# Kernel optimization log

Measured on AMD Instinct MI355X. Metric: run time of the kernel, lower is better.

The kernel has to match this reference:

```python
import jax, jax.numpy as jnp
import numpy as np
import math

NUM_HEAD = 4
GROUPS = 32
EPS = 1e-5


def setup_inputs() -> dict:
    key = jax.random.key(0)
    k1, k2, k3 = jax.random.split(key, 3)
    B, C, H, W = 2, 256, 64, 64
    x = jax.random.normal(k1, (B, C, H, W), dtype=jnp.float32)
    gn_w = jnp.ones((C,), dtype=jnp.float32)
    gn_b = jnp.zeros((C,), dtype=jnp.float32)
    # scaling_init 'u' with scale=1: bound = sqrt(3*2/(fan_in+fan_out))
    fan = (C + 3 * C) / 2
    bound_qkv = math.sqrt(3.0 / fan)
    qkv_w = jax.random.uniform(k2, (3 * C, C), dtype=jnp.float32, minval=-bound_qkv, maxval=bound_qkv)
    bound_o = math.sqrt(3e-10 / C)
    o_w = jax.random.uniform(k3, (C, C), dtype=jnp.float32, minval=-bound_o, maxval=bound_o)
    o_b = jnp.zeros((C,), dtype=jnp.float32)
    return {"x": x, "gn_w": gn_w, "gn_b": gn_b, "qkv_w": qkv_w, "o_w": o_w, "o_b": o_b}


def _group_norm(x, w, b):
    B, C, H, W = x.shape
    xg = x.reshape(B, GROUPS, C // GROUPS, H, W)
    mean = xg.mean(axis=(2, 3, 4), keepdims=True)
    var = xg.var(axis=(2, 3, 4), keepdims=True)
    xn = ((xg - mean) * jax.lax.rsqrt(var + EPS)).reshape(B, C, H, W)
    return xn * w[None, :, None, None] + b[None, :, None, None]


def reference(x, gn_w, gn_b, qkv_w, o_w, o_b):
    B, C, H, W = x.shape
    hd = C // NUM_HEAD
    S = H * W
    norm = _group_norm(x, gn_w, gn_b)
    # 1x1 conv (no bias) == channel matmul
    qkv = jnp.einsum('oc,bchw->bohw', qkv_w, norm)
    qkv = qkv.reshape(B, NUM_HEAD, 3 * hd, S)
    q, k, v = jnp.split(qkv, 3, axis=2)  # each [B, nh, hd, S]
    scale = 1.0 / math.sqrt(C)  # note: sqrt(C), not sqrt(head_dim), per source
    attn = jnp.einsum('bncs,bnct->bnst', q, k) * scale  # [B, nh, S, S]
    attn = jax.nn.softmax(attn, axis=-1)
    out = jnp.einsum('bnst,bnct->bncs', attn, v).reshape(B, C, H, W)
    out = jnp.einsum('oc,bchw->bohw', o_w, out) + o_b[None, :, None, None]
    return out + x
```

## Files before the change

kernel.cpp:

```cpp
#include <hip/hip_runtime.h>
#include <hip/hip_bf16.h>

typedef __hip_bfloat16 bf16;
typedef short short8 __attribute__((ext_vector_type(8)));
typedef float f32x4 __attribute__((ext_vector_type(4)));

__device__ __forceinline__ float b2f(bf16 v) { return __bfloat162float(v); }

__device__ __forceinline__ unsigned short f2bf(float x) {
  unsigned u = __builtin_bit_cast(unsigned, x);
  unsigned r = u + 0x7fffu + ((u >> 16) & 1u);
  return (unsigned short)(r >> 16);
}
__device__ __forceinline__ unsigned pk2(float a, float b) {
  return (unsigned)f2bf(a) | ((unsigned)f2bf(b) << 16);
}
__device__ __forceinline__ unsigned pk2t(float a, float b) {
  return __builtin_amdgcn_perm(__builtin_bit_cast(unsigned, b),
                               __builtin_bit_cast(unsigned, a), 0x07060302u);
}
__device__ __forceinline__ float rd(const void* p, size_t i, int is32) {
  return is32 ? ((const float*)p)[i] : b2f(((const bf16*)p)[i]);
}
__device__ __forceinline__ float blo(unsigned w) {
  return __builtin_bit_cast(float, w << 16);
}
__device__ __forceinline__ float bhi(unsigned w) {
  return __builtin_bit_cast(float, w & 0xffff0000u);
}
__device__ __forceinline__ float fexp2(float x) {
  return __builtin_amdgcn_exp2f(x);
}

#define CQ 0.09016844005556022f

__global__ void __launch_bounds__(256) detect_kernel(const void* __restrict__ x,
                                                     int* __restrict__ flag) {
  __shared__ int cnt[256];
  const bf16* xb = (const bf16*)x;
  int c = 0;
  for (int i = threadIdx.x; i < 4096; i += 256) {
    float v = fabsf(b2f(xb[2 * i]));
    if (v >= 0.0009765625f && v <= 1024.0f) c++;
  }
  cnt[threadIdx.x] = c;
  __syncthreads();
  for (int off = 128; off > 0; off >>= 1) {
    if (threadIdx.x < off) cnt[threadIdx.x] += cnt[threadIdx.x + off];
    __syncthreads();
  }
  if (threadIdx.x == 0) *flag = (cnt[0] < 2048) ? 1 : 0;
}

__global__ void __launch_bounds__(256) pre1_kernel(
    const void* __restrict__ x, const void* __restrict__ gn_w,
    const void* __restrict__ gn_b, const int* __restrict__ flag,
    float* __restrict__ scale, float* __restrict__ shift,
    short* __restrict__ xT) {
  __shared__ __align__(16) float F[64][72];
  const int t = threadIdx.x;
  const int is32 = *flag;
  if (blockIdx.x < 512) {
    const int bx = blockIdx.x;
    const int b = bx >> 8, rest = bx & 255;
    const int s0 = (rest >> 2) * 64, c0 = (rest & 3) * 64;
    if (is32) {
      const float* xp = (const float*)x;
#pragma unroll
      for (int k = 0; k < 4; k++) {
        int idx = k * 256 + t, cl = idx >> 4, c4 = idx & 15;
        float4 v = *(const float4*)&xp[(size_t)(b * 256 + c0 + cl) * 4096 + s0 +
                                       c4 * 4];
        *(float4*)&F[cl][c4 * 4] = v;
      }
    } else {
      const bf16* xp = (const bf16*)x;
#pragma unroll
      for (int k = 0; k < 2; k++) {
        int idx = k * 256 + t, cl = idx >> 3, c8 = idx & 7;
        uint4 u = *(const uint4*)&xp[(size_t)(b * 256 + c0 + cl) * 4096 + s0 +
                                     c8 * 8];
        float4 f0, f1;
        f0.x = blo(u.x); f0.y = bhi(u.x); f0.z = blo(u.y); f0.w = bhi(u.y);
        f1.x = blo(u.z); f1.y = bhi(u.z); f1.z = blo(u.w); f1.w = bhi(u.w);
        *(float4*)&F[cl][c8 * 8] = f0;
        *(float4*)&F[cl][c8 * 8 + 4] = f1;
      }
    }
    __syncthreads();
#pragma unroll
    for (int k = 0; k < 8; k++) {
      int idx = k * 256 + t;
      int sl = idx >> 5, c2 = (idx & 31) * 2;
      unsigned u = pk2(F[c2][sl], F[c2 + 1][sl]);
      *(unsigned*)&xT[((size_t)b * 4096 + s0 + sl) * 256 + c0 + c2] = u;
    }
  } else {
    const int idx0 = blockIdx.x - 512;
    const int b = idx0 >> 5, g = idx0 & 31;
    const size_t base = (size_t)(b * 256 + g * 8) * 4096;
    float s = 0.f, ss = 0.f;
    if (is32) {
      const float4* p = (const float4*)((const float*)x + base);
      for (int i = t; i < 8192; i += 256) {
        float4 v = p[i];
        s += (v.x + v.y) + (v.z + v.w);
        ss += v.x * v.x + v.y * v.y + v.z * v.z + v.w * v.w;
      }
    } else {
      const uint4* p = (const uint4*)((const bf16*)x + base);
      for (int i = t; i < 4096; i += 256) {
        uint4 u = p[i];
#pragma unroll
        for (int k = 0; k < 4; k++) {
          unsigned w = (&u.x)[k];
          float lo = blo(w), hi = bhi(w);
          s += lo + hi;
          ss += lo * lo + hi * hi;
        }
      }
    }
    float* rs = &F[0][0];
    float* rq = rs + 256;
    rs[t] = s;
    rq[t] = ss;
    __syncthreads();
    for (int off = 128; off > 0; off >>= 1) {
      if (t < off) {
        rs[t] += rs[t + off];
        rq[t] += rq[t + off];
      }
      __syncthreads();
    }
    if (t < 8) {
      const float inv_n = 1.f / 32768.f;
      float mean = rs[0] * inv_n;
      float var = rq[0] * inv_n - mean * mean;
      float rstd = rsqrtf(var + 1e-5f);
      int c = g * 8 + t;
      float sc = rd(gn_w, c, is32) * rstd;
      scale[b * 256 + c] = sc;
      shift[b * 256 + c] = rd(gn_b, c, is32) - mean * sc;
    }
  }
}

__global__ void __launch_bounds__(256) pre2_kernel(
    const void* __restrict__ qkv_w, const void* __restrict__ o_w,
    const void* __restrict__ o_b, const float* __restrict__ scale,
    const float* __restrict__ shift, const int* __restrict__ flag,
    short* __restrict__ W2, float* __restrict__ bias2, short* __restrict__ owb,
    float* __restrict__ obf) {
  const int is32 = *flag;
  if (blockIdx.x < 192) {
    const int b = blockIdx.y;
    const int o = blockIdx.x * 4 + (threadIdx.x >> 6);
    const int lane = threadIdx.x & 63;
    const float f = (o % 192 < 64) ? CQ : 1.0f;
    float w[4], acc = 0.f;
#pragma unroll
    for (int k = 0; k < 4; k++) {
      int c = lane * 4 + k;
      w[k] = rd(qkv_w, (size_t)o * 256 + c, is32);
      acc += w[k] * shift[b * 256 + c];
      w[k] = w[k] * scale[b * 256 + c] * f;
    }
#pragma unroll
    for (int m = 1; m < 64; m <<= 1) acc += __shfl_xor(acc, m);
    if (lane == 0) bias2[b * 768 + o] = acc * f;
    uint2 u;
    u.x = pk2(w[0], w[1]);
    u.y = pk2(w[2], w[3]);
    *(uint2*)&W2[((size_t)b * 768 + o) * 256 + lane * 4] = u;
  } else if (blockIdx.y == 0) {
    int bx = blockIdx.x - 192;
    int i = (bx * 256 + threadIdx.x) * 4;
    uint2 u;
    u.x = pk2(rd(o_w, i, is32), rd(o_w, i + 1, is32));
    u.y = pk2(rd(o_w, i + 2, is32), rd(o_w, i + 3, is32));
    *(uint2*)&owb[i] = u;
    if (bx == 0) obf[threadIdx.x] = rd(o_b, threadIdx.x, is32);
  }
}

__global__ void __launch_bounds__(256) gemm_qkv_kernel(
    const short* __restrict__ xT, const short* __restrict__ W2,
    const float* __restrict__ bias2, short* __restrict__ qT,
    short* __restrict__ kF, short* __restrict__ vF) {
  __shared__ __align__(16) short lds[128 * 72 + 64 * 72];
  short* At = lds;
  short* Bt = lds + 128 * 72;
  const int t = threadIdx.x;
  const int wave = t >> 6, lane = t & 63;
  const int ln = lane & 15, quad = lane >> 4;
  const int s0 = blockIdx.x * 128, by = blockIdx.y, b = blockIdx.z;
  const int o0 = by * 64;
  const short* xg = xT + ((size_t)b * 4096 + s0) * 256;
  const short* wg = W2 + ((size_t)b * 768 + o0) * 256;

  f32x4 acc[2][4];
#pragma unroll
  for (int mt = 0; mt < 2; mt++)
#pragma unroll
    for (int nt = 0; nt < 4; nt++) {
      f32x4 z = {0.f, 0.f, 0.f, 0.f};
      acc[mt][nt] = z;
    }

  for (int kt = 0; kt < 4; kt++) {
    __syncthreads();
    {
      int r = t >> 1, ch = t & 1;
#pragma unroll
      for (int j = 0; j < 4; j++)
        *(uint4*)&At[r * 72 + ch * 32 + j * 8] =
            *(const uint4*)&xg[(size_t)r * 256 + kt * 64 + ch * 32 + j * 8];
    }
    {
      int r = t >> 2, cq = t & 3;
#pragma unroll
      for (int j = 0; j < 2; j++)
        *(uint4*)&Bt[r * 72 + cq * 16 + j * 8] =
            *(const uint4*)&wg[(size_t)r * 256 + kt * 64 + cq * 16 + j * 8];
    }
    __syncthreads();
#pragma unroll
    for (int kd = 0; kd < 2; kd++) {
      short8 a[2], bb[4];
#pragma unroll
      for (int mt = 0; mt < 2; mt++)
        a[mt] = *(const short8*)&At[(wave * 32 + mt * 16 + ln) * 72 + kd * 32 +
                                    quad * 8];
#pragma unroll
      for (int nt = 0; nt < 4; nt++)
        bb[nt] = *(const short8*)&Bt[(nt * 16 + ln) * 72 + kd * 32 + quad * 8];
#pragma unroll
      for (int mt = 0; mt < 2; mt++)
#pragma unroll
        for (int nt = 0; nt < 4; nt++)
          acc[mt][nt] = __builtin_amdgcn_mfma_f32_16x16x32_bf16(
              a[mt], bb[nt], acc[mt][nt], 0, 0, 0);
    }
  }

  const int h = by / 3, seg = by % 3;
  const size_t bh = (size_t)b * 4 + h;
  __syncthreads();
  if (seg != 2) {
    short* T = At;
#pragma unroll
    for (int mt = 0; mt < 2; mt++)
#pragma unroll
      for (int nt = 0; nt < 4; nt++)
#pragma unroll
        for (int r = 0; r < 4; r++)
          T[(wave * 32 + mt * 16 + quad * 4 + r) * 72 + nt * 16 + ln] =
              (short)f2bf(acc[mt][nt][r] + bias2[b * 768 + o0 + nt * 16 + ln]);
    __syncthreads();
    if (seg == 0) {
      short* dst = qT + (bh * 4096 + s0) * 64;
      int r = t >> 1, ch = t & 1;
#pragma unroll
      for (int j = 0; j < 2; j++)
        *(uint4*)&dst[r * 64 + ch * 32 + j * 8] =
            *(const uint4*)&T[r * 72 + ch * 32 + j * 8];
    } else {
      short* dstf = kF + bh * 262144;
#pragma unroll
      for (int c = 0; c < 4; c++) {
        int cid = wave * 4 + c;
        int tile = cid >> 1, kd = cid & 1;
        short8 v =
            *(const short8*)&T[(tile * 16 + ln) * 72 + kd * 32 + quad * 8];
        *(short8*)&dstf[(size_t)((s0 / 16 + tile) * 2 + kd) * 512 + lane * 8] =
            v;
      }
    }
  } else {
    short* T2 = At;
#pragma unroll
    for (int mt = 0; mt < 2; mt++)
#pragma unroll
      for (int nt = 0; nt < 4; nt++) {
        float bv = bias2[b * 768 + o0 + nt * 16 + ln];
        uint2 u;
        u.x = pk2(acc[mt][nt][0] + bv, acc[mt][nt][1] + bv);
        u.y = pk2(acc[mt][nt][2] + bv, acc[mt][nt][3] + bv);
        *(uint2*)&T2[(nt * 16 + ln) * 132 + wave * 32 + mt * 16 + quad * 4] = u;
      }
    __syncthreads();
    short* dstf = vF + bh * 262144;
#pragma unroll
    for (int c = 0; c < 4; c++) {
      int cid = wave * 4 + c;
      int ktl = cid >> 3, rem = cid & 7, dt = rem >> 1, kc = rem & 1;
      short8 v = *(const short8*)&T2[(dt * 16 + ln) * 132 + ktl * 64 + kc * 32 +
                                     quad * 8];
      *(short8*)&dstf[(size_t)(((s0 / 64 + ktl) * 4 + dt) * 2 + kc) * 512 +
                      lane * 8] = v;
    }
  }
}

__global__ void __launch_bounds__(256, 2) flash_kernel(
    const short* __restrict__ qT, const short* __restrict__ kF,
    const short* __restrict__ vF, short* __restrict__ attT) {
  __shared__ float smem[4 * 64 * 34];
  const int t = threadIdx.x;
  const int wave = t >> 6, lane = t & 63;
  const int ln = lane & 15, quad = lane >> 4;
  const int L = blockIdx.x;
  const int bh = L & 7;
  const int b = bh >> 2, h = bh & 3;
  const int q0 = (L >> 3) * 32;

  const short* qg = qT + ((size_t)bh * 4096 + q0) * 64;
  const short* kf = kF + (size_t)bh * 262144;
  const short* vf = vF + (size_t)bh * 262144;

  short8 qf[2][2];
#pragma unroll
  for (int qt = 0; qt < 2; qt++)
#pragma unroll
    for (int kd = 0; kd < 2; kd++)
      qf[qt][kd] =
          *(const short8*)&qg[(qt * 16 + ln) * 64 + kd * 32 + quad * 8];

  f32x4 ot[2][4];
#pragma unroll
  for (int qt = 0; qt < 2; qt++)
#pragma unroll
    for (int dt = 0; dt < 4; dt++) {
      f32x4 z = {0.f, 0.f, 0.f, 0.f};
      ot[qt][dt] = z;
    }
  float lres[2] = {0.f, 0.f};

  auto LOADKV = [&](short8(&ka)[4][2], short8(&va)[4][2], int it) {
    const short* kb = kf + (size_t)(wave * 64 + it * 4) * 1024;
#pragma unroll
    for (int ct = 0; ct < 4; ct++)
#pragma unroll
      for (int kd = 0; kd < 2; kd++)
        ka[ct][kd] = *(const short8*)&kb[(ct * 2 + kd) * 512 + lane * 8];
    const short* vb = vf + (size_t)(wave * 16 + it) * 4096;
#pragma unroll
    for (int dt = 0; dt < 4; dt++)
#pragma unroll
      for (int kc = 0; kc < 2; kc++)
        va[dt][kc] = *(const short8*)&vb[(dt * 2 + kc) * 512 + lane * 8];
  };

  auto STEP = [&](const short8(&ka)[4][2], const short8(&va)[4][2]) {
    f32x4 st[2][4];
#pragma unroll
    for (int qt = 0; qt < 2; qt++)
#pragma unroll
      for (int ct = 0; ct < 4; ct++) {
        f32x4 z = {0.f, 0.f, 0.f, 0.f};
        st[qt][ct] = z;
      }
#pragma unroll
    for (int kd = 0; kd < 2; kd++)
#pragma unroll
      for (int ct = 0; ct < 4; ct++) {
        st[0][ct] = __builtin_amdgcn_mfma_f32_16x16x32_bf16(
            ka[ct][kd], qf[0][kd], st[0][ct], 0, 0, 0);
        st[1][ct] = __builtin_amdgcn_mfma_f32_16x16x32_bf16(
            ka[ct][kd], qf[1][kd], st[1][ct], 0, 0, 0);
      }
    unsigned pk[2][4][2];
#pragma unroll
    for (int qt = 0; qt < 2; qt++) {
      float sum = 0.f;
#pragma unroll
      for (int ct = 0; ct < 4; ct++) {
        float p0 = fexp2(st[qt][ct][0]);
        float p1 = fexp2(st[qt][ct][1]);
        float p2 = fexp2(st[qt][ct][2]);
        float p3 = fexp2(st[qt][ct][3]);
        sum += (p0 + p1) + (p2 + p3);
        pk[qt][ct][0] = pk2t(p0, p1);
        pk[qt][ct][1] = pk2t(p2, p3);
      }
      lres[qt] += sum;
    }
#pragma unroll
    for (int kc = 0; kc < 2; kc++) {
      const int tt = kc * 2 + (quad >> 1);
      const int qs = (quad & 1) * 2;
#pragma unroll
      for (int qt = 0; qt < 2; qt++) {
        union {
          unsigned u[4];
          short8 s;
        } bu;
        bu.u[0] = (unsigned)__shfl((int)pk[qt][tt][0], qs * 16 + ln);
        bu.u[1] = (unsigned)__shfl((int)pk[qt][tt][1], qs * 16 + ln);
        bu.u[2] = (unsigned)__shfl((int)pk[qt][tt][0], (qs + 1) * 16 + ln);
        bu.u[3] = (unsigned)__shfl((int)pk[qt][tt][1], (qs + 1) * 16 + ln);
#pragma unroll
        for (int dt = 0; dt < 4; dt++)
          ot[qt][dt] = __builtin_amdgcn_mfma_f32_16x16x32_bf16(
              va[dt][kc], bu.s, ot[qt][dt], 0, 0, 0);
      }
    }
  };

  short8 kaA[4][2], vaA[4][2], kaB[4][2], vaB[4][2];
  LOADKV(kaA, vaA, 0);
#pragma unroll 1
  for (int it = 0; it < 16; it += 2) {
    LOADKV(kaB, vaB, it + 1);
    STEP(kaA, vaA);
    if (it < 14) LOADKV(kaA, vaA, it + 2);
    STEP(kaB, vaB);
  }

#pragma unroll
  for (int qt = 0; qt < 2; qt++) {
    lres[qt] += __shfl_xor(lres[qt], 16);
    lres[qt] += __shfl_xor(lres[qt], 32);
  }
  float* my = smem + (wave * 64 + lane) * 34;
#pragma unroll
  for (int qt = 0; qt < 2; qt++) {
#pragma unroll
    for (int dt = 0; dt < 4; dt++)
      *(f32x4*)&my[qt * 16 + dt * 4] = ot[qt][dt];
    my[32 + qt] = lres[qt];
  }
  __syncthreads();

#pragma unroll
  for (int qt = 0; qt < 2; qt++) {
    float lf = 0.f;
    f32x4 of = {0.f, 0.f, 0.f, 0.f};
#pragma unroll
    for (int w = 0; w < 4; w++) {
      const float* pw = smem + (w * 64 + lane) * 34;
      lf += pw[32 + qt];
      f32x4 o = *(const f32x4*)&pw[qt * 16 + wave * 4];
#pragma unroll
      for (int r = 0; r < 4; r++) of[r] += o[r];
    }
    float invl = 1.f / lf;
    int s = q0 + qt * 16 + ln;
    short* ap =
        attT + ((size_t)b * 4096 + s) * 256 + h * 64 + wave * 16 + quad * 4;
    uint2 u;
    u.x = pk2(of[0] * invl, of[1] * invl);
    u.y = pk2(of[2] * invl, of[3] * invl);
    *(uint2*)ap = u;
  }
}

__global__ void __launch_bounds__(256) gemm_o_kernel(
    const short* __restrict__ owb, const short* __restrict__ attT,
    const float* __restrict__ obf, const void* __restrict__ xres,
    void* __restrict__ out, const int* __restrict__ flag) {
  __shared__ __align__(16) float ldsf[64 * 130];
  short* Bt = (short*)ldsf;
  short* At = Bt + 128 * 72;
  const int t = threadIdx.x;
  const int wave = t >> 6, lane = t & 63;
  const int ln = lane & 15, quad = lane >> 4;
  const int s0 = blockIdx.x * 128, o0 = blockIdx.y * 64, b = blockIdx.z;
  const short* ag = attT + ((size_t)b * 4096 + s0) * 256;

  f32x4 acc[4][2];
#pragma unroll
  for (int mt = 0; mt < 4; mt++)
#pragma unroll
    for (int nt = 0; nt < 2; nt++) {
      f32x4 z = {0.f, 0.f, 0.f, 0.f};
      acc[mt][nt] = z;
    }

  for (int kt = 0; kt < 4; kt++) {
    __syncthreads();
    {
      int r = t >> 1, ch = t & 1;
#pragma unroll
      for (int j = 0; j < 4; j++)
        *(uint4*)&Bt[r * 72 + ch * 32 + j * 8] =
            *(const uint4*)&ag[(size_t)r * 256 + kt * 64 + ch * 32 + j * 8];
    }
    {
      int r = t >> 2, cq = t & 3;
#pragma unroll
      for (int j = 0; j < 2; j++)
        *(uint4*)&At[r * 72 + cq * 16 + j * 8] =
            *(const uint4*)&owb[(size_t)(o0 + r) * 256 + kt * 64 + cq * 16 +
                                j * 8];
    }
    __syncthreads();
#pragma unroll
    for (int kd = 0; kd < 2; kd++) {
      short8 a[4], bb[2];
#pragma unroll
      for (int mt = 0; mt < 4; mt++)
        a[mt] = *(const short8*)&At[(mt * 16 + ln) * 72 + kd * 32 + quad * 8];
#pragma unroll
      for (int nt = 0; nt < 2; nt++)
        bb[nt] = *(const short8*)&Bt[(wave * 32 + nt * 16 + ln) * 72 + kd * 32 +
                                     quad * 8];
#pragma unroll
      for (int mt = 0; mt < 4; mt++)
#pragma unroll
        for (int nt = 0; nt < 2; nt++)
          acc[mt][nt] = __builtin_amdgcn_mfma_f32_16x16x32_bf16(
              a[mt], bb[nt], acc[mt][nt], 0, 0, 0);
    }
  }
  __syncthreads();
#pragma unroll
  for (int mt = 0; mt < 4; mt++)
#pragma unroll
    for (int nt = 0; nt < 2; nt++)
#pragma unroll
      for (int r = 0; r < 4; r++)
        ldsf[(mt * 16 + quad * 4 + r) * 130 + wave * 32 + nt * 16 + ln] =
            acc[mt][nt][r];
  __syncthreads();

  const int is32 = *flag;
#pragma unroll
  for (int j = 0; j < 8; j++) {
    int ol = j * 8 + (t >> 5);
    int sl = (t & 31) * 4;
    f32x4 v = *(const f32x4*)&ldsf[ol * 130 + sl];
    int o = o0 + ol;
    float bv = obf[o];
    size_t base = ((size_t)b * 256 + o) * 4096 + s0 + sl;
    if (is32) {
      const float4 rr = *(const float4*)&((const float*)xres)[base];
      float4 w;
      w.x = v[0] + bv + rr.x;
      w.y = v[1] + bv + rr.y;
      w.z = v[2] + bv + rr.z;
      w.w = v[3] + bv + rr.w;
      *(float4*)&((float*)out)[base] = w;
    } else {
      const uint2 rr = *(const uint2*)&((const bf16*)xres)[base];
      uint2 w;
      w.x = pk2(v[0] + bv + blo(rr.x), v[1] + bv + bhi(rr.x));
      w.y = pk2(v[2] + bv + blo(rr.y), v[3] + bv + bhi(rr.y));
      *(uint2*)&((bf16*)out)[base] = w;
    }
  }
}

extern "C" void kernel_launch(void* const* d_in, const int* in_sizes, int n_in,
                              void* d_out, int out_size, void* d_ws,
                              size_t ws_size, hipStream_t stream) {
  float* ws = (float*)d_ws;
  int* flag = (int*)ws;
  float* scale = ws + 256;
  float* shift = ws + 768;
  float* bias2 = ws + 1280;
  float* obf = ws + 2816;
  short* owb = (short*)(ws + 3072);
  short* W2 = (short*)(ws + 35840);
  short* xT = (short*)(ws + 232448);
  short* qT = (short*)(ws + 1281024);
  short* kF = (short*)(ws + 2329600);
  short* vF = (short*)(ws + 3378176);
  short* attT = (short*)(ws + 4426752);

  detect_kernel<<<1, 256, 0, stream>>>(d_in[0], flag);
  pre1_kernel<<<576, 256, 0, stream>>>(d_in[0], d_in[1], d_in[2], flag, scale,
                                       shift, xT);
  pre2_kernel<<<dim3(256, 2), 256, 0, stream>>>(d_in[3], d_in[4], d_in[5],
                                                scale, shift, flag, W2, bias2,
                                                owb, obf);
  gemm_qkv_kernel<<<dim3(32, 12, 2), 256, 0, stream>>>(xT, W2, bias2, qT, kF,
                                                       vF);
  flash_kernel<<<1024, 256, 0, stream>>>(qT, kF, vF, attT);
  gemm_o_kernel<<<dim3(32, 4, 2), 256, 0, stream>>>(owb, attT, obf, d_in[0],
                                                    d_out, flag);
}
```

Measured before the change: 187.4 us.

## Preload full weight tile and register-prefetch activations in QKV and output GEMMs

Both projection GEMMs now load the entire 256-wide weight tile into LDS once, then prefetch the next activation K-slice into registers while MFMAs run on the current slice. The output GEMM also halves its spatial tile to 64, doubling the grid, with one accumulator column per wave. The goal is to hide global-load latency behind compute and to give the small output GEMM more blocks. The cost is more LDS per block and extra barriers per K step.

New measurement: 211.5 us. 12.9% more time.

```diff
diff --git a/kernel.cpp b/kernel.cpp
--- a/kernel.cpp
+++ b/kernel.cpp
@@ -187,9 +187,9 @@
     const short* __restrict__ xT, const short* __restrict__ W2,
     const float* __restrict__ bias2, short* __restrict__ qT,
     short* __restrict__ kF, short* __restrict__ vF) {
-  __shared__ __align__(16) short lds[128 * 72 + 64 * 72];
-  short* At = lds;
-  short* Bt = lds + 128 * 72;
+  __shared__ __align__(16) short lds[64 * 264 + 128 * 72];
+  short* Bt = lds;
+  short* At = lds + 64 * 264;
   const int t = threadIdx.x;
   const int wave = t >> 6, lane = t & 63;
   const int ln = lane & 15, quad = lane >> 4;
@@ -198,6 +198,23 @@
   const short* xg = xT + ((size_t)b * 4096 + s0) * 256;
   const short* wg = W2 + ((size_t)b * 768 + o0) * 256;
 
+  {
+    int r = t >> 2, c0q = (t & 3) * 8;
+#pragma unroll
+    for (int j = 0; j < 8; j++)
+      *(uint4*)&Bt[r * 264 + (c0q + j) * 8] =
+          *(const uint4*)&wg[r * 256 + (c0q + j) * 8];
+  }
+  uint4 ra[4];
+  const int ar = t >> 1, ach = t & 1;
+#pragma unroll
+  for (int j = 0; j < 4; j++)
+    ra[j] = *(const uint4*)&xg[(size_t)ar * 256 + ach * 32 + j * 8];
+#pragma unroll
+  for (int j = 0; j < 4; j++)
+    *(uint4*)&At[ar * 72 + ach * 32 + j * 8] = ra[j];
+  __syncthreads();
+
   f32x4 acc[2][4];
 #pragma unroll
   for (int mt = 0; mt < 2; mt++)
@@ -208,22 +225,12 @@
     }
 
   for (int kt = 0; kt < 4; kt++) {
-    __syncthreads();
-    {
-      int r = t >> 1, ch = t & 1;
+    if (kt < 3) {
 #pragma unroll
       for (int j = 0; j < 4; j++)
-        *(uint4*)&At[r * 72 + ch * 32 + j * 8] =
-            *(const uint4*)&xg[(size_t)r * 256 + kt * 64 + ch * 32 + j * 8];
-    }
-    {
-      int r = t >> 2, cq = t & 3;
-#pragma unroll
-      for (int j = 0; j < 2; j++)
-        *(uint4*)&Bt[r * 72 + cq * 16 + j * 8] =
-            *(const uint4*)&wg[(size_t)r * 256 + kt * 64 + cq * 16 + j * 8];
-    }
-    __syncthreads();
+        ra[j] = *(const uint4*)&xg[(size_t)ar * 256 + (kt + 1) * 64 + ach * 32 +
+                                   j * 8];
+    }
 #pragma unroll
     for (int kd = 0; kd < 2; kd++) {
       short8 a[2], bb[4];
@@ -233,13 +240,21 @@
                                     quad * 8];
 #pragma unroll
       for (int nt = 0; nt < 4; nt++)
-        bb[nt] = *(const short8*)&Bt[(nt * 16 + ln) * 72 + kd * 32 + quad * 8];
+        bb[nt] = *(const short8*)&Bt[(nt * 16 + ln) * 264 + kt * 64 + kd * 32 +
+                                     quad * 8];
 #pragma unroll
       for (int mt = 0; mt < 2; mt++)
 #pragma unroll
         for (int nt = 0; nt < 4; nt++)
           acc[mt][nt] = __builtin_amdgcn_mfma_f32_16x16x32_bf16(
               a[mt], bb[nt], acc[mt][nt], 0, 0, 0);
+    }
+    if (kt < 3) {
+      __syncthreads();
+#pragma unroll
+      for (int j = 0; j < 4; j++)
+        *(uint4*)&At[ar * 72 + ach * 32 + j * 8] = ra[j];
+      __syncthreads();
     }
   }
 
@@ -459,77 +474,83 @@
     const short* __restrict__ owb, const short* __restrict__ attT,
     const float* __restrict__ obf, const void* __restrict__ xres,
     void* __restrict__ out, const int* __restrict__ flag) {
-  __shared__ __align__(16) float ldsf[64 * 130];
-  short* Bt = (short*)ldsf;
-  short* At = Bt + 128 * 72;
+  __shared__ __align__(16) float ldsf[10752];
+  short* At = (short*)ldsf;
+  short* Bs = At + 64 * 264;
   const int t = threadIdx.x;
   const int wave = t >> 6, lane = t & 63;
   const int ln = lane & 15, quad = lane >> 4;
-  const int s0 = blockIdx.x * 128, o0 = blockIdx.y * 64, b = blockIdx.z;
+  const int s0 = blockIdx.x * 64, o0 = blockIdx.y * 64, b = blockIdx.z;
   const short* ag = attT + ((size_t)b * 4096 + s0) * 256;
 
-  f32x4 acc[4][2];
+  {
+    int r = t >> 2, c0q = (t & 3) * 8;
+#pragma unroll
+    for (int j = 0; j < 8; j++)
+      *(uint4*)&At[r * 264 + (c0q + j) * 8] =
+          *(const uint4*)&owb[(size_t)(o0 + r) * 256 + (c0q + j) * 8];
+  }
+  uint4 rb[2];
+  const int br = t >> 2, bc = t & 3;
+#pragma unroll
+  for (int j = 0; j < 2; j++)
+    rb[j] = *(const uint4*)&ag[(size_t)br * 256 + (bc * 2 + j) * 8];
+#pragma unroll
+  for (int j = 0; j < 2; j++)
+    *(uint4*)&Bs[br * 72 + (bc * 2 + j) * 8] = rb[j];
+  __syncthreads();
+
+  f32x4 acc[4];
+#pragma unroll
+  for (int mt = 0; mt < 4; mt++) {
+    f32x4 z = {0.f, 0.f, 0.f, 0.f};
+    acc[mt] = z;
+  }
+
+  for (int kt = 0; kt < 4; kt++) {
+    if (kt < 3) {
+#pragma unroll
+      for (int j = 0; j < 2; j++)
+        rb[j] = *(const uint4*)&ag[(size_t)br * 256 + (kt + 1) * 64 +
+                                   (bc * 2 + j) * 8];
+    }
+#pragma unroll
+    for (int kd = 0; kd < 2; kd++) {
+      short8 a[4];
+#pragma unroll
+      for (int mt = 0; mt < 4; mt++)
+        a[mt] = *(const short8*)&At[(mt * 16 + ln) * 264 + kt * 64 + kd * 32 +
+                                    quad * 8];
+      short8 bb = *(const short8*)&Bs[(wave * 16 + ln) * 72 + kd * 32 +
+                                      quad * 8];
+#pragma unroll
+      for (int mt = 0; mt < 4; mt++)
+        acc[mt] = __builtin_amdgcn_mfma_f32_16x16x32_bf16(a[mt], bb, acc[mt],
+                                                          0, 0, 0);
+    }
+    if (kt < 3) {
+      __syncthreads();
+#pragma unroll
+      for (int j = 0; j < 2; j++)
+        *(uint4*)&Bs[br * 72 + (bc * 2 + j) * 8] = rb[j];
+      __syncthreads();
+    }
+  }
+
+  __syncthreads();
 #pragma unroll
   for (int mt = 0; mt < 4; mt++)
 #pragma unroll
-    for (int nt = 0; nt < 2; nt++) {
-      f32x4 z = {0.f, 0.f, 0.f, 0.f};
-      acc[mt][nt] = z;
-    }
-
-  for (int kt = 0; kt < 4; kt++) {
-    __syncthreads();
-    {
-      int r = t >> 1, ch = t & 1;
-#pragma unroll
-      for (int j = 0; j < 4; j++)
-        *(uint4*)&Bt[r * 72 + ch * 32 + j * 8] =
-            *(const uint4*)&ag[(size_t)r * 256 + kt * 64 + ch * 32 + j * 8];
-    }
-    {
-      int r = t >> 2, cq = t & 3;
-#pragma unroll
-      for (int j = 0; j < 2; j++)
-        *(uint4*)&At[r * 72 + cq * 16 + j * 8] =
-            *(const uint4*)&owb[(size_t)(o0 + r) * 256 + kt * 64 + cq * 16 +
-                                j * 8];
-    }
-    __syncthreads();
-#pragma unroll
-    for (int kd = 0; kd < 2; kd++) {
-      short8 a[4], bb[2];
-#pragma unroll
-      for (int mt = 0; mt < 4; mt++)
-        a[mt] = *(const short8*)&At[(mt * 16 + ln) * 72 + kd * 32 + quad * 8];
-#pragma unroll
-      for (int nt = 0; nt < 2; nt++)
-        bb[nt] = *(const short8*)&Bt[(wave * 32 + nt * 16 + ln) * 72 + kd * 32 +
-                                     quad * 8];
-#pragma unroll
-      for (int mt = 0; mt < 4; mt++)
-#pragma unroll
-        for (int nt = 0; nt < 2; nt++)
-          acc[mt][nt] = __builtin_amdgcn_mfma_f32_16x16x32_bf16(
-              a[mt], bb[nt], acc[mt][nt], 0, 0, 0);
-    }
-  }
+    for (int r = 0; r < 4; r++)
+      ldsf[(mt * 16 + quad * 4 + r) * 66 + wave * 16 + ln] = acc[mt][r];
   __syncthreads();
-#pragma unroll
-  for (int mt = 0; mt < 4; mt++)
-#pragma unroll
-    for (int nt = 0; nt < 2; nt++)
-#pragma unroll
-      for (int r = 0; r < 4; r++)
-        ldsf[(mt * 16 + quad * 4 + r) * 130 + wave * 32 + nt * 16 + ln] =
-            acc[mt][nt][r];
-  __syncthreads();
 
   const int is32 = *flag;
 #pragma unroll
-  for (int j = 0; j < 8; j++) {
-    int ol = j * 8 + (t >> 5);
-    int sl = (t & 31) * 4;
-    f32x4 v = *(const f32x4*)&ldsf[ol * 130 + sl];
+  for (int j = 0; j < 4; j++) {
+    int ol = j * 16 + (t >> 4);
+    int sl = (t & 15) * 4;
+    f32x4 v = *(const f32x4*)&ldsf[ol * 66 + sl];
     int o = o0 + ol;
     float bv = obf[o];
     size_t base = ((size_t)b * 256 + o) * 4096 + s0 + sl;
@@ -577,6 +598,6 @@
   gemm_qkv_kernel<<<dim3(32, 12, 2), 256, 0, stream>>>(xT, W2, bias2, qT, kF,
                                                        vF);
   flash_kernel<<<1024, 256, 0, stream>>>(qT, kF, vF, attT);
-  gemm_o_kernel<<<dim3(32, 4, 2), 256, 0, stream>>>(owb, attT, obf, d_in[0],
+  gemm_o_kernel<<<dim3(64, 4, 2), 256, 0, stream>>>(owb, attT, obf, d_in[0],
                                                     d_out, flag);
 }
```
